# Kernel tuning notes

Measured on AMD Instinct MI355X. Metric: run time of the kernel, lower is better.

The kernel has to match this reference:

```python
import jax, jax.numpy as jnp
import numpy as np

N_NODES = 50000
N_EDGES = 1600000
IN_CH = 128
HEADS = 4
HEAD_DIM = 32  # out_channels // heads = 128 // 4
NEG_SLOPE = 0.2


def setup_inputs() -> dict:
    key = jax.random.key(0)
    ks = jax.random.split(key, 6)
    x = jax.random.normal(ks[0], (N_NODES, IN_CH), dtype=jnp.float32)
    edge_index = jax.random.randint(ks[1], (2, N_EDGES), 0, N_NODES, dtype=jnp.int64)
    W = jax.random.normal(ks[2], (IN_CH, HEADS * HEAD_DIM), dtype=jnp.float32) * 0.1
    att_src = jax.random.normal(ks[3], (HEADS, HEAD_DIM), dtype=jnp.float32) * 0.1
    att_dst = jax.random.normal(ks[4], (HEADS, HEAD_DIM), dtype=jnp.float32) * 0.1
    bias = jax.random.normal(ks[5], (HEADS * HEAD_DIM,), dtype=jnp.float32) * 0.1
    return {"x": x, "edge_index": edge_index, "W": W,
            "att_src": att_src, "att_dst": att_dst, "bias": bias}


def reference(x, edge_index, W, att_src, att_dst, bias):
    N = x.shape[0]
    # linear projection, split heads: [N, H, C]
    h = (x @ W).reshape(N, HEADS, HEAD_DIM)
    # per-node attention logits: [N, H]
    a_src = jnp.einsum('nhc,hc->nh', h, att_src)
    a_dst = jnp.einsum('nhc,hc->nh', h, att_dst)
    # add self loops (PyG default)
    loops = jnp.arange(N, dtype=edge_index.dtype)
    src = jnp.concatenate([edge_index[0], loops])  # message source j
    dst = jnp.concatenate([edge_index[1], loops])  # message target i
    # edge attention scores: [E_total, H]
    alpha = jax.nn.leaky_relu(a_src[src] + a_dst[dst], NEG_SLOPE)
    # segment softmax over incoming edges per destination node
    amax = jax.ops.segment_max(alpha, dst, num_segments=N)
    alpha = jnp.exp(alpha - amax[dst])
    denom = jax.ops.segment_sum(alpha, dst, num_segments=N)
    alpha = alpha / (denom[dst] + 1e-16)
    # weighted scatter-aggregate: [N, H, C]
    msg = h[src] * alpha[:, :, None]
    out = jax.ops.segment_sum(msg, dst, num_segments=N)
    out = out.reshape(N, HEADS * HEAD_DIM) + bias
    return jax.nn.elu(out)
```

## Files before the change

kernel.cpp:

```cpp
#include <hip/hip_runtime.h>

typedef unsigned short u16;
typedef unsigned int u32;

#define CH 128
#define NHEAD 4
#define NEG_SLOPE 0.2f
#define ROWS_PER_BLOCK 32

#define LOG_NPB 7
#define NPB 128
#define NBMAX 400
#define BCAP 6144
#define KMAX 24
#define GPAD 16
#define BINA_BLOCKS 256

static __device__ __forceinline__ float bitf(u32 i) {
    float f; __builtin_memcpy(&f, &i, 4); return f;
}
static __device__ __forceinline__ float bflo(u32 v) { return bitf(v << 16); }
static __device__ __forceinline__ float bfhi(u32 v) { return bitf(v & 0xffff0000u); }
static __device__ __forceinline__ u16 f2bf(float f) {
    u32 i; __builtin_memcpy(&i, &f, 4);
    return (u16)((i + 0x7fffu + ((i >> 16) & 1u)) >> 16);
}
static __device__ __forceinline__ float lrelu(float v) { return v > 0.f ? v : NEG_SLOPE * v; }

static __device__ __forceinline__ int ei_at(const int* __restrict__ ei, int mode32, size_t idx) {
    return mode32 ? ei[idx] : ei[2 * idx];
}

__global__ __launch_bounds__(256) void binA_kernel(
    const int* __restrict__ ei, int* __restrict__ gcur, u32* __restrict__ rec,
    int E, int NB)
{
    __shared__ int hist[NBMAX];
    __shared__ int hbase[NBMAX];
    __shared__ int hcur[NBMAX];
    const int tid = threadIdx.x;
    const int mode32 = __syncthreads_or(ei[2 * tid + 1] != 0);
    for (int b = tid; b < NB; b += 256) { hist[b] = 0; hcur[b] = 0; }
    __syncthreads();
    const int chunk = (E + BINA_BLOCKS - 1) / BINA_BLOCKS;
    const int beg0 = blockIdx.x * chunk;
    const int end0 = min(E, beg0 + chunk);
#pragma unroll 4
    for (int e = beg0 + tid; e < end0; e += 256) {
        int dj = ei_at(ei, mode32, (size_t)E + e);
        atomicAdd(&hist[dj >> LOG_NPB], 1);
    }
    __syncthreads();
    for (int b = tid; b < NB; b += 256) {
        int c = hist[b];
        hbase[b] = c ? atomicAdd(&gcur[b * GPAD], c) : 0;
    }
    __syncthreads();
#pragma unroll 4
    for (int e = beg0 + tid; e < end0; e += 256) {
        int dj = ei_at(ei, mode32, (size_t)E + e);
        int sj = ei_at(ei, mode32, (size_t)e);
        int bkt = dj >> LOG_NPB;
        int r = atomicAdd(&hcur[bkt], 1);
        int pos = hbase[bkt] + r;
        if (pos < BCAP)
            rec[(size_t)bkt * BCAP + pos] = ((u32)sj << LOG_NPB) | (u32)(dj & (NPB - 1));
    }
}

union SMem {
    struct { float xs[ROWS_PER_BLOCK][CH]; u32 Wbf[CH][CH / 2]; } g;
    struct { int outb[BCAP]; int lcnt[NPB]; int lsc[NPB]; int lcur[NPB]; } b;
};

__global__ __launch_bounds__(256) void gemmbinB_kernel(
    const float* __restrict__ x, const float* __restrict__ W,
    const float* __restrict__ att_src, const float* __restrict__ att_dst,
    u16* __restrict__ h, float* __restrict__ asrc, float* __restrict__ adst, int N,
    const int* __restrict__ gcur, const u32* __restrict__ rec,
    int* __restrict__ csr, int* __restrict__ begA, int* __restrict__ degA, int NB)
{
    __shared__ SMem sm;
    const int tid = threadIdx.x;

    if ((int)blockIdx.x < NB) {
        int* outb = sm.b.outb;
        int* lcnt = sm.b.lcnt;
        int* lsc  = sm.b.lsc;
        int* lcur = sm.b.lcur;
        const int bkt = blockIdx.x;
        int cnt0 = gcur[bkt * GPAD];
        cnt0 = cnt0 < BCAP ? cnt0 : BCAP;
        const size_t rbase = (size_t)bkt * BCAP;

        if (tid < NPB) { lcnt[tid] = 0; lcur[tid] = 0; }

        u32 rc[KMAX];
#pragma unroll
        for (int k = 0; k < KMAX; ++k) {
            int i = tid + k * 256;
            rc[k] = (i < cnt0) ? rec[rbase + i] : 0xffffffffu;
        }
        __syncthreads();
#pragma unroll
        for (int k = 0; k < KMAX; ++k)
            if (rc[k] != 0xffffffffu) atomicAdd(&lcnt[rc[k] & (NPB - 1)], 1);
        __syncthreads();
        if (tid < NPB) lsc[tid] = lcnt[tid];
        __syncthreads();
        for (int o = 1; o < NPB; o <<= 1) {
            int v = (tid < NPB && tid >= o) ? lsc[tid - o] : 0;
            __syncthreads();
            if (tid < NPB) lsc[tid] += v;
            __syncthreads();
        }
#pragma unroll
        for (int k = 0; k < KMAX; ++k) {
            if (rc[k] != 0xffffffffu) {
                int local = rc[k] & (NPB - 1);
                int r = atomicAdd(&lcur[local], 1);
                int slot = (lsc[local] - lcnt[local]) + r;
                outb[slot] = (int)(rc[k] >> LOG_NPB);
            }
        }
        __syncthreads();
        for (int i = tid; i < cnt0; i += 256)
            csr[rbase + i] = outb[i];
        if (tid < NPB) {
            int node = (bkt << LOG_NPB) + tid;
            if (node < N) {
                begA[node] = (int)rbase + (lsc[tid] - lcnt[tid]);
                degA[node] = lcnt[tid];
            }
        }
        return;
    }

    const int gb = blockIdx.x - NB;
    const int r0b = gb * ROWS_PER_BLOCK;
    {
#pragma unroll
        for (int i = 0; i < 16; ++i) {
            int f = tid + i * 256;
            int row = f >> 5;
            int col = (f & 31) * 4;
            float4 w4 = *(const float4*)(W + (size_t)row * CH + col);
            sm.g.Wbf[row][(col >> 1)]     = (u32)f2bf(w4.x) | ((u32)f2bf(w4.y) << 16);
            sm.g.Wbf[row][(col >> 1) + 1] = (u32)f2bf(w4.z) | ((u32)f2bf(w4.w) << 16);
        }
#pragma unroll
        for (int i = 0; i < 4; ++i) {
            int f = tid + i * 256;
            int row = f >> 5;
            int col = (f & 31) * 4;
            if (r0b + row < N)
                *(float4*)&sm.g.xs[row][col] = *(const float4*)(x + (size_t)(r0b + row) * CH + col);
        }
    }
    __syncthreads();

    const int lane = tid & 63;
    const int wave = tid >> 6;
    const int c0 = lane * 2;
    const int head = lane >> 4;
    const float as0 = att_src[c0], as1 = att_src[c0 + 1];
    const float ad0 = att_dst[c0], ad1 = att_dst[c0 + 1];
    const int rw = wave * 8;

    float acc[8][2];
#pragma unroll
    for (int r = 0; r < 8; ++r) { acc[r][0] = 0.f; acc[r][1] = 0.f; }

#pragma unroll 4
    for (int k4 = 0; k4 < 32; ++k4) {
        const int k = k4 * 4;
        u32 p0 = sm.g.Wbf[k + 0][lane];
        u32 p1 = sm.g.Wbf[k + 1][lane];
        u32 p2 = sm.g.Wbf[k + 2][lane];
        u32 p3 = sm.g.Wbf[k + 3][lane];
        float w00 = bflo(p0), w01 = bfhi(p0);
        float w10 = bflo(p1), w11 = bfhi(p1);
        float w20 = bflo(p2), w21 = bfhi(p2);
        float w30 = bflo(p3), w31 = bfhi(p3);
#pragma unroll
        for (int r = 0; r < 8; ++r) {
            float4 xv = *(const float4*)&sm.g.xs[rw + r][k];
            acc[r][0] = fmaf(xv.x, w00, acc[r][0]);
            acc[r][1] = fmaf(xv.x, w01, acc[r][1]);
            acc[r][0] = fmaf(xv.y, w10, acc[r][0]);
            acc[r][1] = fmaf(xv.y, w11, acc[r][1]);
            acc[r][0] = fmaf(xv.z, w20, acc[r][0]);
            acc[r][1] = fmaf(xv.z, w21, acc[r][1]);
            acc[r][0] = fmaf(xv.w, w30, acc[r][0]);
            acc[r][1] = fmaf(xv.w, w31, acc[r][1]);
        }
    }
#pragma unroll
    for (int r = 0; r < 8; ++r) {
        int row = r0b + rw + r;
        float sdot = acc[r][0] * as0 + acc[r][1] * as1;
        float ddot = acc[r][0] * ad0 + acc[r][1] * ad1;
#pragma unroll
        for (int o = 1; o < 16; o <<= 1) {
            sdot += __shfl_xor(sdot, o, 64);
            ddot += __shfl_xor(ddot, o, 64);
        }
        if (row < N) {
            u32 hp = (u32)f2bf(acc[r][0]) | ((u32)f2bf(acc[r][1]) << 16);
            *(u32*)(h + (size_t)row * CH + c0) = hp;
            if ((lane & 15) == 0) {
                asrc[row * NHEAD + head] = sdot;
                adst[row * NHEAD + head] = ddot;
            }
        }
    }
}

__global__ __launch_bounds__(256) void agg_kernel(
    const u16* __restrict__ h, const float* __restrict__ asrc, const float* __restrict__ adst,
    const int* __restrict__ begA, const int* __restrict__ degA, const int* __restrict__ csr,
    const float* __restrict__ bias, float* __restrict__ out, int N)
{
    const int lane = threadIdx.x & 63;
    const int wave = threadIdx.x >> 6;
    const int node = blockIdx.x * 4 + wave;
    if (node >= N) return;
    const int g = lane >> 4;
    const int l = lane & 15;
    const int c8 = l * 8;
    const int head = l >> 2;
    const int beg = begA[node];
    const int end = beg + degA[node];
    const float4 ad4 = *(const float4*)(adst + node * 4);
    const float adh = (head == 0) ? ad4.x : (head == 1) ? ad4.y : (head == 2) ? ad4.z : ad4.w;
    const float4 asl = *(const float4*)(asrc + node * 4);
    const float aslh = (head == 0) ? asl.x : (head == 1) ? asl.y : (head == 2) ? asl.z : asl.w;
    const float mh = lrelu(aslh + adh);

    float acc[8];
#pragma unroll
    for (int k = 0; k < 8; ++k) acc[k] = 0.f;
    float s = 0.f;

    int e = beg + g;
    if (e < end) {
        uint4 hC[4]; float aC[4];
#pragma unroll
        for (int i = 0; i < 4; ++i) {
            int ei = e + 4 * i;
            int j = csr[ei];
            j = ((u32)j < (u32)N) ? j : 0;
            float a = asrc[j * NHEAD + head];
            aC[i] = (ei < end) ? a : -1e30f;
            hC[i] = *(const uint4*)(h + (size_t)j * CH + c8);
        }
        for (;;) {
            const int ebase = e + 16;
            uint4 hP[4]; float aP[4];
#pragma unroll
            for (int i = 0; i < 4; ++i) {
                int ei = ebase + 4 * i;
                int j = csr[ei];
                j = ((u32)j < (u32)N) ? j : 0;
                float a = asrc[j * NHEAD + head];
                aP[i] = (ei < end) ? a : -1e30f;
                hP[i] = *(const uint4*)(h + (size_t)j * CH + c8);
            }
#pragma unroll
            for (int i = 0; i < 4; ++i) {
                float w = __expf(lrelu(aC[i] + adh) - mh);
                s += w;
                acc[0] = fmaf(w, bflo(hC[i].x), acc[0]);
                acc[1] = fmaf(w, bfhi(hC[i].x), acc[1]);
                acc[2] = fmaf(w, bflo(hC[i].y), acc[2]);
                acc[3] = fmaf(w, bfhi(hC[i].y), acc[3]);
                acc[4] = fmaf(w, bflo(hC[i].z), acc[4]);
                acc[5] = fmaf(w, bfhi(hC[i].z), acc[5]);
                acc[6] = fmaf(w, bflo(hC[i].w), acc[6]);
                acc[7] = fmaf(w, bfhi(hC[i].w), acc[7]);
            }
#pragma unroll
            for (int i = 0; i < 4; ++i) { aC[i] = aP[i]; hC[i] = hP[i]; }
            e = ebase;
            if (e >= end) break;
        }
    }
    if (g == 0) {
        s += 1.0f;
        uint4 hv = *(const uint4*)(h + (size_t)node * CH + c8);
        acc[0] += bflo(hv.x);
        acc[1] += bfhi(hv.x);
        acc[2] += bflo(hv.y);
        acc[3] += bfhi(hv.y);
        acc[4] += bflo(hv.z);
        acc[5] += bfhi(hv.z);
        acc[6] += bflo(hv.w);
        acc[7] += bfhi(hv.w);
    }
#pragma unroll
    for (int o = 16; o < 64; o <<= 1) {
        s += __shfl_xor(s, o, 64);
#pragma unroll
        for (int k = 0; k < 8; ++k) acc[k] += __shfl_xor(acc[k], o, 64);
    }
    if (g == 0) {
        const float inv = 1.f / (s + 1e-16f);
        float o0[8];
#pragma unroll
        for (int k = 0; k < 8; ++k) {
            float v = acc[k] * inv + bias[c8 + k];
            o0[k] = v > 0.f ? v : __expf(v) - 1.f;
        }
        float4 lo = make_float4(o0[0], o0[1], o0[2], o0[3]);
        float4 hi = make_float4(o0[4], o0[5], o0[6], o0[7]);
        *(float4*)(out + (size_t)node * CH + c8) = lo;
        *(float4*)(out + (size_t)node * CH + c8 + 4) = hi;
    }
}

extern "C" void kernel_launch(void* const* d_in, const int* in_sizes, int n_in,
                              void* d_out, int out_size, void* d_ws, size_t ws_size,
                              hipStream_t stream)
{
    const float* x       = (const float*)d_in[0];
    const int*   ei      = (const int*)d_in[1];
    const float* W       = (const float*)d_in[2];
    const float* att_src = (const float*)d_in[3];
    const float* att_dst = (const float*)d_in[4];
    const float* bias    = (const float*)d_in[5];
    float* out = (float*)d_out;
    const int N = in_sizes[0] / CH;
    const int E = in_sizes[1] / 2;
    const int NB = (N + NPB - 1) / NPB;

    char* p = (char*)d_ws;
    auto alloc = [&](size_t bytes) { char* r = p; p += (bytes + 255) & ~(size_t)255; return r; };
    u16*   h    = (u16*)alloc((size_t)N * CH * 2);
    float* asrc = (float*)alloc((size_t)N * NHEAD * 4);
    float* adst = (float*)alloc((size_t)N * NHEAD * 4);
    int*   gcur = (int*)alloc((size_t)NB * GPAD * 4);
    u32*   rec  = (u32*)alloc((size_t)NB * BCAP * 4);
    int*   csr  = (int*)alloc((size_t)NB * BCAP * 4 + 256);
    int*   begA = (int*)alloc((size_t)N * 4);
    int*   degA = (int*)alloc((size_t)N * 4);

    const int gemmBlocks = (N + ROWS_PER_BLOCK - 1) / ROWS_PER_BLOCK;
    hipMemsetAsync(gcur, 0, (size_t)NB * GPAD * 4, stream);
    binA_kernel<<<BINA_BLOCKS, 256, 0, stream>>>(ei, gcur, rec, E, NB);
    gemmbinB_kernel<<<NB + gemmBlocks, 256, 0, stream>>>(
        x, W, att_src, att_dst, h, asrc, adst, N, gcur, rec, csr, begA, degA, NB);
    agg_kernel<<<(N + 3) / 4, 256, 0, stream>>>(h, asrc, adst, begA, degA, csr, bias, out, N);
}
```

Before: 220.0 us.

## Split GEMM tiles across both binning kernels and widen phase-A binning grid

```diff
diff --git a/kernel.cpp b/kernel.cpp
--- a/kernel.cpp
+++ b/kernel.cpp
@@ -14,7 +14,8 @@
 #define BCAP 6144
 #define KMAX 24
 #define GPAD 16
-#define BINA_BLOCKS 256
+#define BINA_BLOCKS 2048
+#define KA 4
 
 static __device__ __forceinline__ float bitf(u32 i) {
     float f; __builtin_memcpy(&f, &i, 4); return f;
@@ -31,54 +32,169 @@
     return mode32 ? ei[idx] : ei[2 * idx];
 }
 
-__global__ __launch_bounds__(256) void binA_kernel(
+static __device__ __forceinline__ void gemm_tile(
+    const float* __restrict__ x, const float* __restrict__ W,
+    const float* __restrict__ att_src, const float* __restrict__ att_dst,
+    u16* __restrict__ h, float* __restrict__ asrc, float* __restrict__ adst,
+    int N, int r0b, float (*xs)[CH], u32 (*Wbf)[CH / 2], int tid)
+{
+#pragma unroll
+    for (int i = 0; i < 16; ++i) {
+        int f = tid + i * 256;
+        int row = f >> 5;
+        int col = (f & 31) * 4;
+        float4 w4 = *(const float4*)(W + (size_t)row * CH + col);
+        Wbf[row][(col >> 1)]     = (u32)f2bf(w4.x) | ((u32)f2bf(w4.y) << 16);
+        Wbf[row][(col >> 1) + 1] = (u32)f2bf(w4.z) | ((u32)f2bf(w4.w) << 16);
+    }
+#pragma unroll
+    for (int i = 0; i < 4; ++i) {
+        int f = tid + i * 256;
+        int row = f >> 5;
+        int col = (f & 31) * 4;
+        if (r0b + row < N)
+            *(float4*)&xs[row][col] = *(const float4*)(x + (size_t)(r0b + row) * CH + col);
+    }
+    __syncthreads();
+
+    const int lane = tid & 63;
+    const int wave = tid >> 6;
+    const int c0 = lane * 2;
+    const int head = lane >> 4;
+    const float as0 = att_src[c0], as1 = att_src[c0 + 1];
+    const float ad0 = att_dst[c0], ad1 = att_dst[c0 + 1];
+    const int rw = wave * 8;
+
+    float acc[8][2];
+#pragma unroll
+    for (int r = 0; r < 8; ++r) { acc[r][0] = 0.f; acc[r][1] = 0.f; }
+
+#pragma unroll 4
+    for (int k4 = 0; k4 < 32; ++k4) {
+        const int k = k4 * 4;
+        u32 p0 = Wbf[k + 0][lane];
+        u32 p1 = Wbf[k + 1][lane];
+        u32 p2 = Wbf[k + 2][lane];
+        u32 p3 = Wbf[k + 3][lane];
+        float w00 = bflo(p0), w01 = bfhi(p0);
+        float w10 = bflo(p1), w11 = bfhi(p1);
+        float w20 = bflo(p2), w21 = bfhi(p2);
+        float w30 = bflo(p3), w31 = bfhi(p3);
+#pragma unroll
+        for (int r = 0; r < 8; ++r) {
+            float4 xv = *(const float4*)&xs[rw + r][k];
+            acc[r][0] = fmaf(xv.x, w00, acc[r][0]);
+            acc[r][1] = fmaf(xv.x, w01, acc[r][1]);
+            acc[r][0] = fmaf(xv.y, w10, acc[r][0]);
+            acc[r][1] = fmaf(xv.y, w11, acc[r][1]);
+            acc[r][0] = fmaf(xv.z, w20, acc[r][0]);
+            acc[r][1] = fmaf(xv.z, w21, acc[r][1]);
+            acc[r][0] = fmaf(xv.w, w30, acc[r][0]);
+            acc[r][1] = fmaf(xv.w, w31, acc[r][1]);
+        }
+    }
+#pragma unroll
+    for (int r = 0; r < 8; ++r) {
+        int row = r0b + rw + r;
+        float sdot = acc[r][0] * as0 + acc[r][1] * as1;
+        float ddot = acc[r][0] * ad0 + acc[r][1] * ad1;
+#pragma unroll
+        for (int o = 1; o < 16; o <<= 1) {
+            sdot += __shfl_xor(sdot, o, 64);
+            ddot += __shfl_xor(ddot, o, 64);
+        }
+        if (row < N) {
+            u32 hp = (u32)f2bf(acc[r][0]) | ((u32)f2bf(acc[r][1]) << 16);
+            *(u32*)(h + (size_t)row * CH + c0) = hp;
+            if ((lane & 15) == 0) {
+                asrc[row * NHEAD + head] = sdot;
+                adst[row * NHEAD + head] = ddot;
+            }
+        }
+    }
+}
+
+union SMem {
+    struct { float xs[ROWS_PER_BLOCK][CH]; u32 Wbf[CH][CH / 2]; } g;
+    struct { int hist[NBMAX]; int hbase[NBMAX]; int hcur[NBMAX]; } a;
+    struct { int outb[BCAP]; int lcnt[NPB]; int lsc[NPB]; int lcur[NPB]; } b;
+};
+
+__global__ __launch_bounds__(256) void binAgemm_kernel(
+    const float* __restrict__ x, const float* __restrict__ W,
+    const float* __restrict__ att_src, const float* __restrict__ att_dst,
+    u16* __restrict__ h, float* __restrict__ asrc, float* __restrict__ adst, int N,
     const int* __restrict__ ei, int* __restrict__ gcur, u32* __restrict__ rec,
     int E, int NB)
 {
-    __shared__ int hist[NBMAX];
-    __shared__ int hbase[NBMAX];
-    __shared__ int hcur[NBMAX];
+    __shared__ SMem sm;
     const int tid = threadIdx.x;
-    const int mode32 = __syncthreads_or(ei[2 * tid + 1] != 0);
-    for (int b = tid; b < NB; b += 256) { hist[b] = 0; hcur[b] = 0; }
-    __syncthreads();
-    const int chunk = (E + BINA_BLOCKS - 1) / BINA_BLOCKS;
-    const int beg0 = blockIdx.x * chunk;
-    const int end0 = min(E, beg0 + chunk);
-#pragma unroll 4
-    for (int e = beg0 + tid; e < end0; e += 256) {
-        int dj = ei_at(ei, mode32, (size_t)E + e);
-        atomicAdd(&hist[dj >> LOG_NPB], 1);
-    }
-    __syncthreads();
-    for (int b = tid; b < NB; b += 256) {
-        int c = hist[b];
-        hbase[b] = c ? atomicAdd(&gcur[b * GPAD], c) : 0;
-    }
-    __syncthreads();
-#pragma unroll 4
-    for (int e = beg0 + tid; e < end0; e += 256) {
-        int dj = ei_at(ei, mode32, (size_t)E + e);
-        int sj = ei_at(ei, mode32, (size_t)e);
-        int bkt = dj >> LOG_NPB;
-        int r = atomicAdd(&hcur[bkt], 1);
-        int pos = hbase[bkt] + r;
-        if (pos < BCAP)
-            rec[(size_t)bkt * BCAP + pos] = ((u32)sj << LOG_NPB) | (u32)(dj & (NPB - 1));
-    }
-}
-
-union SMem {
-    struct { float xs[ROWS_PER_BLOCK][CH]; u32 Wbf[CH][CH / 2]; } g;
-    struct { int outb[BCAP]; int lcnt[NPB]; int lsc[NPB]; int lcur[NPB]; } b;
-};
-
-__global__ __launch_bounds__(256) void gemmbinB_kernel(
+
+    if (blockIdx.x < BINA_BLOCKS) {
+        int* hist  = sm.a.hist;
+        int* hbase = sm.a.hbase;
+        int* hcur  = sm.a.hcur;
+        const int mode32 = __syncthreads_or(ei[2 * tid + 1] != 0);
+        for (int b = tid; b < NB; b += 256) { hist[b] = 0; hcur[b] = 0; }
+        __syncthreads();
+        const int chunk = (E + BINA_BLOCKS - 1) / BINA_BLOCKS;
+        const int beg0 = blockIdx.x * chunk;
+        const int end0 = min(E, beg0 + chunk);
+        int djr[KA], sjr[KA];
+#pragma unroll
+        for (int k = 0; k < KA; ++k) {
+            int e = beg0 + tid + k * 256;
+            bool v = e < end0;
+            djr[k] = v ? ei_at(ei, mode32, (size_t)E + e) : -1;
+            sjr[k] = v ? ei_at(ei, mode32, (size_t)e) : 0;
+        }
+#pragma unroll
+        for (int k = 0; k < KA; ++k)
+            if (djr[k] >= 0) atomicAdd(&hist[djr[k] >> LOG_NPB], 1);
+        for (int e = beg0 + tid + KA * 256; e < end0; e += 256) {
+            int dj = ei_at(ei, mode32, (size_t)E + e);
+            atomicAdd(&hist[dj >> LOG_NPB], 1);
+        }
+        __syncthreads();
+        for (int b = tid; b < NB; b += 256) {
+            int c = hist[b];
+            hbase[b] = c ? atomicAdd(&gcur[b * GPAD], c) : 0;
+        }
+        __syncthreads();
+#pragma unroll
+        for (int k = 0; k < KA; ++k) {
+            if (djr[k] >= 0) {
+                int bkt = djr[k] >> LOG_NPB;
+                int r = atomicAdd(&hcur[bkt], 1);
+                int pos = hbase[bkt] + r;
+                if (pos < BCAP)
+                    rec[(size_t)bkt * BCAP + pos] =
+                        ((u32)sjr[k] << LOG_NPB) | (u32)(djr[k] & (NPB - 1));
+            }
+        }
+        for (int e = beg0 + tid + KA * 256; e < end0; e += 256) {
+            int dj = ei_at(ei, mode32, (size_t)E + e);
+            int sj = ei_at(ei, mode32, (size_t)e);
+            int bkt = dj >> LOG_NPB;
+            int r = atomicAdd(&hcur[bkt], 1);
+            int pos = hbase[bkt] + r;
+            if (pos < BCAP)
+                rec[(size_t)bkt * BCAP + pos] = ((u32)sj << LOG_NPB) | (u32)(dj & (NPB - 1));
+        }
+        return;
+    }
+
+    gemm_tile(x, W, att_src, att_dst, h, asrc, adst, N,
+              (int)(blockIdx.x - BINA_BLOCKS) * ROWS_PER_BLOCK, sm.g.xs, sm.g.Wbf, tid);
+}
+
+__global__ __launch_bounds__(256) void binBgemm_kernel(
     const float* __restrict__ x, const float* __restrict__ W,
     const float* __restrict__ att_src, const float* __restrict__ att_dst,
     u16* __restrict__ h, float* __restrict__ asrc, float* __restrict__ adst, int N,
     const int* __restrict__ gcur, const u32* __restrict__ rec,
-    int* __restrict__ csr, int* __restrict__ begA, int* __restrict__ degA, int NB)
+    int* __restrict__ csr, int* __restrict__ begA, int* __restrict__ degA,
+    int NB, int G1)
 {
     __shared__ SMem sm;
     const int tid = threadIdx.x;
@@ -136,84 +252,8 @@
         return;
     }
 
-    const int gb = blockIdx.x - NB;
-    const int r0b = gb * ROWS_PER_BLOCK;
-    {
-#pragma unroll
-        for (int i = 0; i < 16; ++i) {
-            int f = tid + i * 256;
-            int row = f >> 5;
-            int col = (f & 31) * 4;
-            float4 w4 = *(const float4*)(W + (size_t)row * CH + col);
-            sm.g.Wbf[row][(col >> 1)]     = (u32)f2bf(w4.x) | ((u32)f2bf(w4.y) << 16);
-            sm.g.Wbf[row][(col >> 1) + 1] = (u32)f2bf(w4.z) | ((u32)f2bf(w4.w) << 16);
-        }
-#pragma unroll
-        for (int i = 0; i < 4; ++i) {
-            int f = tid + i * 256;
-            int row = f >> 5;
-            int col = (f & 31) * 4;
-            if (r0b + row < N)
-                *(float4*)&sm.g.xs[row][col] = *(const float4*)(x + (size_t)(r0b + row) * CH + col);
-        }
-    }
-    __syncthreads();
-
-    const int lane = tid & 63;
-    const int wave = tid >> 6;
-    const int c0 = lane * 2;
-    const int head = lane >> 4;
-    const float as0 = att_src[c0], as1 = att_src[c0 + 1];
-    const float ad0 = att_dst[c0], ad1 = att_dst[c0 + 1];
-    const int rw = wave * 8;
-
-    float acc[8][2];
-#pragma unroll
-    for (int r = 0; r < 8; ++r) { acc[r][0] = 0.f; acc[r][1] = 0.f; }
-
-#pragma unroll 4
-    for (int k4 = 0; k4 < 32; ++k4) {
-        const int k = k4 * 4;
-        u32 p0 = sm.g.Wbf[k + 0][lane];
-        u32 p1 = sm.g.Wbf[k + 1][lane];
-        u32 p2 = sm.g.Wbf[k + 2][lane];
-        u32 p3 = sm.g.Wbf[k + 3][lane];
-        float w00 = bflo(p0), w01 = bfhi(p0);
-        float w10 = bflo(p1), w11 = bfhi(p1);
-        float w20 = bflo(p2), w21 = bfhi(p2);
-        float w30 = bflo(p3), w31 = bfhi(p3);
-#pragma unroll
-        for (int r = 0; r < 8; ++r) {
-            float4 xv = *(const float4*)&sm.g.xs[rw + r][k];
-            acc[r][0] = fmaf(xv.x, w00, acc[r][0]);
-            acc[r][1] = fmaf(xv.x, w01, acc[r][1]);
-            acc[r][0] = fmaf(xv.y, w10, acc[r][0]);
-            acc[r][1] = fmaf(xv.y, w11, acc[r][1]);
-            acc[r][0] = fmaf(xv.z, w20, acc[r][0]);
-            acc[r][1] = fmaf(xv.z, w21, acc[r][1]);
-            acc[r][0] = fmaf(xv.w, w30, acc[r][0]);
-            acc[r][1] = fmaf(xv.w, w31, acc[r][1]);
-        }
-    }
-#pragma unroll
-    for (int r = 0; r < 8; ++r) {
-        int row = r0b + rw + r;
-        float sdot = acc[r][0] * as0 + acc[r][1] * as1;
-        float ddot = acc[r][0] * ad0 + acc[r][1] * ad1;
-#pragma unroll
-        for (int o = 1; o < 16; o <<= 1) {
-            sdot += __shfl_xor(sdot, o, 64);
-            ddot += __shfl_xor(ddot, o, 64);
-        }
-        if (row < N) {
-            u32 hp = (u32)f2bf(acc[r][0]) | ((u32)f2bf(acc[r][1]) << 16);
-            *(u32*)(h + (size_t)row * CH + c0) = hp;
-            if ((lane & 15) == 0) {
-                asrc[row * NHEAD + head] = sdot;
-                adst[row * NHEAD + head] = ddot;
-            }
-        }
-    }
+    gemm_tile(x, W, att_src, att_dst, h, asrc, adst, N,
+              (G1 + (int)blockIdx.x - NB) * ROWS_PER_BLOCK, sm.g.xs, sm.g.Wbf, tid);
 }
 
 __global__ __launch_bounds__(256) void agg_kernel(
@@ -345,9 +385,12 @@
     int*   degA = (int*)alloc((size_t)N * 4);
 
     const int gemmBlocks = (N + ROWS_PER_BLOCK - 1) / ROWS_PER_BLOCK;
+    const int G1 = (gemmBlocks * 3) / 5;
+    const int G2 = gemmBlocks - G1;
     hipMemsetAsync(gcur, 0, (size_t)NB * GPAD * 4, stream);
-    binA_kernel<<<BINA_BLOCKS, 256, 0, stream>>>(ei, gcur, rec, E, NB);
-    gemmbinB_kernel<<<NB + gemmBlocks, 256, 0, stream>>>(
-        x, W, att_src, att_dst, h, asrc, adst, N, gcur, rec, csr, begA, degA, NB);
+    binAgemm_kernel<<<BINA_BLOCKS + G1, 256, 0, stream>>>(
+        x, W, att_src, att_dst, h, asrc, adst, N, ei, gcur, rec, E, NB);
+    binBgemm_kernel<<<NB + G2, 256, 0, stream>>>(
+        x, W, att_src, att_dst, h, asrc, adst, N, gcur, rec, csr, begA, degA, NB, G1);
     agg_kernel<<<(N + 3) / 4, 256, 0, stream>>>(h, asrc, adst, begA, degA, csr, bias, out, N);
 }
```

After: 244.2 us. 1.11x slower.
